# Kernel optimization log

Hardware: AMD Instinct MI355X
Metric: run time of the kernel (lower is better)

## Reference

```python
import jax, jax.numpy as jnp
import numpy as np

N = 50000
E = 800000
EL = 100000
IN_CH = 33
HID = 64
OUT = 128
NTYPES = 311
EMB = 16
COMB = IN_CH - 1 + EMB  # 48


def setup_inputs() -> dict:
    key = jax.random.key(0)
    ks = jax.random.split(key, 24)
    # x: col 0 = node type (integer-valued float), rest = float features
    types = jax.random.randint(ks[0], (N, 1), 0, NTYPES).astype(jnp.float32)
    feats = jax.random.normal(ks[1], (N, IN_CH - 1), dtype=jnp.float32)
    x = jnp.concatenate([types, feats], axis=1)
    edge_index = jax.random.randint(ks[2], (2, E), 0, N, dtype=jnp.int32)
    edge_label_index = jax.random.randint(ks[3], (2, EL), 0, N, dtype=jnp.int32)
    s = 0.05
    inp = {
        'x': x, 'edge_index': edge_index, 'edge_label_index': edge_label_index,
        'emb': jax.random.normal(ks[4], (NTYPES, EMB)) * s,
        'W1': jax.random.normal(ks[5], (COMB, 4 * HID)) * s,
        'a_src1': jax.random.normal(ks[6], (4, HID)) * s,
        'a_dst1': jax.random.normal(ks[7], (4, HID)) * s,
        'b1': jnp.zeros((4 * HID,)),
        'W2': jax.random.normal(ks[8], (4 * HID, 2 * 2 * HID)) * s,
        'a_src2': jax.random.normal(ks[9], (2, 2 * HID)) * s,
        'a_dst2': jax.random.normal(ks[10], (2, 2 * HID)) * s,
        'b2': jnp.zeros((2 * 2 * HID,)),
        'W3': jax.random.normal(ks[11], (4 * HID, OUT)) * s,
        'a_src3': jax.random.normal(ks[12], (1, OUT)) * s,
        'a_dst3': jax.random.normal(ks[13], (1, OUT)) * s,
        'b3': jnp.zeros((OUT,)),
        'Wl1': jax.random.normal(ks[14], (2 * OUT, HID)) * s,
        'bl1': jnp.zeros((HID,)),
        'Wl2': jax.random.normal(ks[15], (HID, 1)) * s,
        'bl2': jnp.zeros((1,)),
        'trans_bias': jax.random.normal(ks[16], (NTYPES, NTYPES)) * s,
    }
    return inp


def _gat(h_in, src, dst, W, a_src, a_dst, b, heads, d_out):
    # linear transform, per-head split
    h = (h_in @ W).reshape(N, heads, d_out)                      # [N,H,D]
    al_s = jnp.einsum('nhd,hd->nh', h, a_src)                    # [N,H]
    al_d = jnp.einsum('nhd,hd->nh', h, a_dst)
    logits = jax.nn.leaky_relu(al_s[src] + al_d[dst], 0.2)       # [E,H]
    m = jax.ops.segment_max(logits, dst, num_segments=N)
    m = jnp.where(jnp.isfinite(m), m, 0.0)
    e = jnp.exp(logits - m[dst])
    denom = jax.ops.segment_sum(e, dst, num_segments=N)
    alpha = e / (denom[dst] + 1e-16)                             # [E,H]
    msg = h[src] * alpha[:, :, None]                             # [E,H,D]
    out = jax.ops.segment_sum(msg, dst, num_segments=N)          # [N,H,D]
    return out.reshape(N, heads * d_out) + b


def reference(x, edge_index, edge_label_index, emb, W1, a_src1, a_dst1, b1,
              W2, a_src2, a_dst2, b2, W3, a_src3, a_dst3, b3,
              Wl1, bl1, Wl2, bl2, trans_bias):
    node_types = x[:, 0].astype(jnp.int32)
    x_comb = jnp.concatenate([emb[node_types], x[:, 1:]], axis=1)  # [N,48]
    # add self loops (PyG GATConv default)
    loops = jnp.arange(N, dtype=edge_index.dtype)
    ei = jnp.concatenate([edge_index, jnp.stack([loops, loops])], axis=1)
    src, dst = ei[0], ei[1]
    z = jax.nn.elu(_gat(x_comb, src, dst, W1, a_src1, a_dst1, b1, 4, HID))
    z = jax.nn.elu(_gat(z, src, dst, W2, a_src2, a_dst2, b2, 2, 2 * HID))
    z = _gat(z, src, dst, W3, a_src3, a_dst3, b3, 1, OUT)
    # decode
    ls, ld = edge_label_index[0], edge_label_index[1]
    ef = jnp.concatenate([z[ls], z[ld]], axis=1)                  # [EL,2*OUT]
    h = jax.nn.relu(ef @ Wl1 + bl1)
    base = h @ Wl2 + bl2                                          # [EL,1]
    bias = trans_bias[node_types[ls], node_types[ld]][:, None]
    return base + bias
```

## Files before the change

kernel.cpp:

```cpp
#include <hip/hip_runtime.h>
#include <hip/hip_bf16.h>

#define NN 50000
#define EE 800000
#define ELN 100000
#define ETOT (EE + NN)
#define NT 311

#define NBUCK ((NN + 127) >> 7)
#define BCAP 3072
#define CHUNK 8192

typedef _Float16 f16;
typedef f16 f16x8 __attribute__((ext_vector_type(8)));
typedef f16 f16x4 __attribute__((ext_vector_type(4)));
typedef f16 f16x2 __attribute__((ext_vector_type(2)));
typedef float f32x4 __attribute__((ext_vector_type(4)));

__global__ __launch_bounds__(256) void k_prepatt(const float* __restrict__ x,
                                                 const float* __restrict__ emb,
                                                 const float* __restrict__ a1ps,
                                                 const float* __restrict__ a1pd,
                                                 f16* __restrict__ xc,
                                                 int* __restrict__ ntypes,
                                                 float* __restrict__ als,
                                                 float* __restrict__ ald)
{
    int gid = blockIdx.x * 256 + threadIdx.x;
    int n = gid >> 6, lane = gid & 63;
    if (n >= NN) return;
    int tpe = (int)x[(size_t)n * 33];
    tpe = tpe < 0 ? 0 : (tpe > NT - 1 ? NT - 1 : tpe);
    if (lane == 0) ntypes[n] = tpe;
    float v;
    if (lane < 16)      v = emb[tpe * 16 + lane];
    else if (lane < 48) v = x[(size_t)n * 33 + 1 + (lane - 16)];
    else                v = 0.f;
    f16 hv = (f16)v;
    xc[(size_t)n * 64 + lane] = hv;
    float xv = (float)hv;
    float ps[4], pd[4];
    #pragma unroll
    for (int h = 0; h < 4; ++h) {
        ps[h] = xv * a1ps[h * 64 + lane];
        pd[h] = xv * a1pd[h * 64 + lane];
    }
    #pragma unroll
    for (int off = 32; off > 0; off >>= 1) {
        #pragma unroll
        for (int h = 0; h < 4; ++h) {
            ps[h] += __shfl_xor(ps[h], off, 64);
            pd[h] += __shfl_xor(pd[h], off, 64);
        }
    }
    if (lane == 0) {
        #pragma unroll
        for (int h = 0; h < 4; ++h) {
            als[n * 4 + h] = ps[h];
            ald[n * 4 + h] = pd[h];
        }
    }
}

__global__ __launch_bounds__(256) void k_cvtall(const float* __restrict__ W1,
                                                const float* __restrict__ W2,
                                                const float* __restrict__ W3,
                                                const float* __restrict__ Wl1,
                                                f16* __restrict__ Wt1,
                                                f16* __restrict__ Wt2,
                                                f16* __restrict__ Wt3,
                                                f16* __restrict__ Wtl)
{
    int idx = blockIdx.x * 256 + threadIdx.x;
    if (idx < 16384) {
        int h = idx >> 12, c = (idx >> 6) & 63, k = idx & 63;
        Wt1[idx] = (k < 48) ? (f16)W1[(size_t)k * 256 + h * 64 + c] : (f16)0.f;
    } else if (idx < 81920) {
        int i = idx - 16384;
        int c = i >> 8, k = i & 255;
        Wt2[i] = (f16)W2[(size_t)k * 256 + c];
    } else if (idx < 114688) {
        int i = idx - 81920;
        int c = i >> 8, k = i & 255;
        Wt3[i] = (f16)W3[(size_t)k * 128 + c];
    } else if (idx < 131072) {
        int i = idx - 114688;
        int c = i >> 8, k = i & 255;
        Wtl[i] = (f16)Wl1[(size_t)k * 64 + c];
    }
}

__global__ __launch_bounds__(256) void k_pre1(const float* __restrict__ W1,
                                              const float* __restrict__ as1,
                                              const float* __restrict__ ad1,
                                              float* __restrict__ a1ps,
                                              float* __restrict__ a1pd)
{
    int t = threadIdx.x;
    int h = t >> 6, k = t & 63;
    float ss = 0.f, sd = 0.f;
    if (k < 48) {
        for (int d = 0; d < 64; ++d) {
            float w = W1[(size_t)k * 256 + h * 64 + d];
            ss += w * as1[h * 64 + d];
            sd += w * ad1[h * 64 + d];
        }
    }
    a1ps[t] = ss;
    a1pd[t] = sd;
}

__global__ __launch_bounds__(256) void k_bucket(const int* __restrict__ ei,
                                                int* __restrict__ bcur,
                                                int2* __restrict__ bbuf)
{
    __shared__ int hist[NBUCK];
    __shared__ int gbase[NBUCK];
    const int t = threadIdx.x;
    for (int i = t; i < NBUCK; i += 256) hist[i] = 0;
    __syncthreads();
    const int e0 = blockIdx.x * CHUNK;
    const int eend = min(e0 + CHUNK, ETOT);
    for (int e = e0 + t; e < eend; e += 256) {
        int dst = (e < EE) ? ei[EE + e] : (e - EE);
        atomicAdd(&hist[dst >> 7], 1);
    }
    __syncthreads();
    for (int i = t; i < NBUCK; i += 256) {
        int c = hist[i];
        gbase[i] = c ? atomicAdd(&bcur[i], c) : 0;
        hist[i] = 0;
    }
    __syncthreads();
    for (int e = e0 + t; e < eend; e += 256) {
        int src, dst;
        if (e < EE) { src = ei[e]; dst = ei[EE + e]; }
        else        { src = e - EE; dst = src; }
        int b = dst >> 7;
        int pos = gbase[b] + atomicAdd(&hist[b], 1);
        if (pos < BCAP)
            bbuf[(size_t)b * BCAP + pos] = make_int2(src, dst);
    }
}

__global__ __launch_bounds__(512) void k_bscan(const int* __restrict__ bcur,
                                               int* __restrict__ boff)
{
    __shared__ int s[512];
    int t = threadIdx.x;
    int v = (t < NBUCK) ? min(bcur[t], BCAP) : 0;
    s[t] = v;
    __syncthreads();
    #pragma unroll
    for (int off = 1; off < 512; off <<= 1) {
        int u = (t >= off) ? s[t - off] : 0;
        __syncthreads();
        s[t] += u;
        __syncthreads();
    }
    if (t < NBUCK) boff[t] = s[t] - v;
    if (t == NBUCK - 1) boff[NBUCK] = s[t];
}

__global__ __launch_bounds__(256) void k_csrb(const int* __restrict__ bcur,
                                              const int* __restrict__ boff,
                                              const int2* __restrict__ bbuf,
                                              int* __restrict__ rowptr,
                                              int* __restrict__ csr,
                                              int* __restrict__ dstarr)
{
    __shared__ int nh[128];
    __shared__ int loff[128];
    __shared__ int ncur[128];
    __shared__ int ssrc[BCAP];
    __shared__ int sdst[BCAP];
    const int b = blockIdx.x;
    const int t = threadIdx.x;
    const int n0 = b << 7;
    const int cnt = min(bcur[b], BCAP);
    const int base = boff[b];
    const size_t bb = (size_t)b * BCAP;
    if (t < 128) { nh[t] = 0; ncur[t] = 0; }
    __syncthreads();
    for (int i = t; i < cnt; i += 256)
        atomicAdd(&nh[bbuf[bb + i].y - n0], 1);
    __syncthreads();
    int myc = (t < 128) ? nh[t] : 0;
    #pragma unroll
    for (int off = 1; off < 128; off <<= 1) {
        int u = (t >= off && t < 128) ? nh[t - off] : 0;
        __syncthreads();
        if (t < 128) nh[t] += u;
        __syncthreads();
    }
    if (t < 128) {
        int ex = nh[t] - myc;
        loff[t] = ex;
        int n = n0 + t;
        if (n < NN) rowptr[n] = base + ex;
    }
    __syncthreads();
    for (int i = t; i < cnt; i += 256) {
        int2 p = bbuf[bb + i];
        int ln = p.y - n0;
        int pos = loff[ln] + atomicAdd(&ncur[ln], 1);
        ssrc[pos] = p.x;
        sdst[pos] = p.y;
    }
    __syncthreads();
    for (int i = t; i < cnt; i += 256) {
        csr[base + i]    = ssrc[i];
        dstarr[base + i] = sdst[i];
    }
    if (b == 0 && t == 0) rowptr[NN] = boff[NBUCK];
}

template<int K, int CN, int H>
__global__ __launch_bounds__(256) void k_gemmh(const f16* __restrict__ A,
                                               const f16* __restrict__ Wt,
                                               f16* __restrict__ O,
                                               int nrows,
                                               const float* __restrict__ asrc,
                                               const float* __restrict__ adst,
                                               float* __restrict__ als,
                                               float* __restrict__ ald)
{
    constexpr int LDA = 40;
    __shared__ f16 As[64 * LDA];
    __shared__ f16 Bs[64 * LDA];
    const int t = threadIdx.x;
    const int w = t >> 6;
    const int lane = t & 63;
    const int m = lane & 15;
    const int quad = lane >> 4;
    const int row0 = blockIdx.x * 64;
    const int col0 = blockIdx.y * 64;
    const int r_st = t >> 2;
    const int seg  = (t & 3) * 8;
    f32x4 acc[4] = {{0.f,0.f,0.f,0.f},{0.f,0.f,0.f,0.f},{0.f,0.f,0.f,0.f},{0.f,0.f,0.f,0.f}};
    for (int k0 = 0; k0 < K; k0 += 32) {
        int gr = row0 + r_st;
        f16x8 av = {0,0,0,0,0,0,0,0};
        if (gr < nrows) av = *(const f16x8*)&A[(size_t)gr * K + k0 + seg];
        *(f16x8*)&As[r_st * LDA + seg] = av;
        f16x8 bv = *(const f16x8*)&Wt[(size_t)(col0 + r_st) * K + k0 + seg];
        *(f16x8*)&Bs[r_st * LDA + seg] = bv;
        __syncthreads();
        f16x8 af = *(const f16x8*)&As[(w * 16 + m) * LDA + quad * 8];
        #pragma unroll
        for (int g = 0; g < 4; ++g) {
            f16x8 bf = *(const f16x8*)&Bs[(g * 16 + m) * LDA + quad * 8];
            acc[g] = __builtin_amdgcn_mfma_f32_16x16x32_f16(af, bf, acc[g], 0, 0, 0);
        }
        __syncthreads();
    }
    #pragma unroll
    for (int g = 0; g < 4; ++g) {
        #pragma unroll
        for (int reg = 0; reg < 4; ++reg) {
            int gr = row0 + w * 16 + quad * 4 + reg;
            int gc = col0 + g * 16 + m;
            if (gr < nrows) O[(size_t)gr * CN + gc] = (f16)acc[g][reg];
        }
    }
    if constexpr (H > 0) {
        constexpr int D = CN / H;
        const int head = col0 / D;
        float ps[4] = {}, pd[4] = {};
        #pragma unroll
        for (int g = 0; g < 4; ++g) {
            int col = col0 + g * 16 + m;
            float a_s = asrc[col], a_d = adst[col];
            #pragma unroll
            for (int reg = 0; reg < 4; ++reg) {
                ps[reg] += acc[g][reg] * a_s;
                pd[reg] += acc[g][reg] * a_d;
            }
        }
        #pragma unroll
        for (int off = 1; off < 16; off <<= 1) {
            #pragma unroll
            for (int reg = 0; reg < 4; ++reg) {
                ps[reg] += __shfl_xor(ps[reg], off, 64);
                pd[reg] += __shfl_xor(pd[reg], off, 64);
            }
        }
        if (m == 0) {
            #pragma unroll
            for (int reg = 0; reg < 4; ++reg) {
                int gr = row0 + w * 16 + quad * 4 + reg;
                if (gr < nrows) {
                    atomicAdd(&als[gr * H + head], ps[reg]);
                    atomicAdd(&ald[gr * H + head], pd[reg]);
                }
            }
        }
    }
}

__global__ __launch_bounds__(256) void k_gemm1h(const f16* __restrict__ A,
                                                const f16* __restrict__ Wt1,
                                                const float* __restrict__ bias,
                                                f16* __restrict__ O,
                                                int nrows)
{
    constexpr int LDA = 40;
    __shared__ f16 As[64 * LDA];
    __shared__ f16 Bs[64 * LDA];
    const int t = threadIdx.x;
    const int w = t >> 6;
    const int lane = t & 63;
    const int m = lane & 15;
    const int quad = lane >> 4;
    const int row0 = blockIdx.x * 64;
    const int head = blockIdx.y;
    const int r_st = t >> 2;
    const int seg  = (t & 3) * 8;
    f32x4 acc[4] = {{0.f,0.f,0.f,0.f},{0.f,0.f,0.f,0.f},{0.f,0.f,0.f,0.f},{0.f,0.f,0.f,0.f}};
    for (int k0 = 0; k0 < 64; k0 += 32) {
        int gr = row0 + r_st;
        f16x8 av = {0,0,0,0,0,0,0,0};
        if (gr < nrows) av = *(const f16x8*)&A[(size_t)gr * 256 + head * 64 + k0 + seg];
        *(f16x8*)&As[r_st * LDA + seg] = av;
        f16x8 bv = *(const f16x8*)&Wt1[(size_t)head * 4096 + (size_t)r_st * 64 + k0 + seg];
        *(f16x8*)&Bs[r_st * LDA + seg] = bv;
        __syncthreads();
        f16x8 af = *(const f16x8*)&As[(w * 16 + m) * LDA + quad * 8];
        #pragma unroll
        for (int g = 0; g < 4; ++g) {
            f16x8 bf = *(const f16x8*)&Bs[(g * 16 + m) * LDA + quad * 8];
            acc[g] = __builtin_amdgcn_mfma_f32_16x16x32_f16(af, bf, acc[g], 0, 0, 0);
        }
        __syncthreads();
    }
    #pragma unroll
    for (int g = 0; g < 4; ++g) {
        #pragma unroll
        for (int reg = 0; reg < 4; ++reg) {
            int gr = row0 + w * 16 + quad * 4 + reg;
            int col = head * 64 + g * 16 + m;
            if (gr < nrows) {
                float v = acc[g][reg] + bias[col];
                v = v > 0.f ? v : (__expf(v) - 1.f);
                O[(size_t)gr * 256 + col] = (f16)v;
            }
        }
    }
}

template<int H>
__global__ __launch_bounds__(256) void k_ew(const int* __restrict__ csr,
                                            const int* __restrict__ dstarr,
                                            const float* __restrict__ als,
                                            const float* __restrict__ ald,
                                            float* __restrict__ earr)
{
    int i = blockIdx.x * 256 + threadIdx.x;
    if (i >= ETOT) return;
    int s = csr[i], d = dstarr[i];
    #pragma unroll
    for (int hh = 0; hh < H; ++hh) {
        float l = als[s * H + hh] + ald[d * H + hh];
        l = l > 0.f ? l : 0.2f * l;
        earr[(size_t)i * H + hh] = __expf(fminf(l, 80.f));
    }
}

__global__ __launch_bounds__(256) void k_aggx(const int* __restrict__ rowptr,
                                              const int* __restrict__ csr,
                                              const float* __restrict__ earr,
                                              const f16* __restrict__ xc,
                                              f16* __restrict__ xagg)
{
    int gid = blockIdx.x * 256 + threadIdx.x;
    int n = gid >> 6, lane = gid & 63;
    if (n >= NN) return;
    int p  = lane >> 5;
    int cb = (lane & 31) * 2;
    int r0 = rowptr[n], r1 = rowptr[n + 1];
    float a0[2] = {}, a1[2] = {}, a2[2] = {}, a3[2] = {};
    float d0 = 0.f, d1 = 0.f, d2 = 0.f, d3 = 0.f;
    int i = r0;
    for (; i + 4 <= r1; i += 4) {
        int i0 = i + p, i1 = i + 2 + p;
        int s0 = csr[i0], s1 = csr[i1];
        float4 e0 = *(const float4*)&earr[(size_t)i0 * 4];
        float4 e1 = *(const float4*)&earr[(size_t)i1 * 4];
        f16x2 x0 = *(const f16x2*)&xc[(size_t)s0 * 64 + cb];
        f16x2 x1 = *(const f16x2*)&xc[(size_t)s1 * 64 + cb];
        #pragma unroll
        for (int j = 0; j < 2; ++j) {
            float v0 = (float)x0[j], v1 = (float)x1[j];
            a0[j] += e0.x * v0 + e1.x * v1;
            a1[j] += e0.y * v0 + e1.y * v1;
            a2[j] += e0.z * v0 + e1.z * v1;
            a3[j] += e0.w * v0 + e1.w * v1;
        }
        d0 += e0.x + e1.x; d1 += e0.y + e1.y;
        d2 += e0.z + e1.z; d3 += e0.w + e1.w;
    }
    for (; i < r1; i += 2) {
        int ii = i + p;
        bool v = ii < r1;
        int s0 = csr[v ? ii : r0];
        float4 e0 = *(const float4*)&earr[(size_t)(v ? ii : r0) * 4];
        if (!v) { e0.x = 0.f; e0.y = 0.f; e0.z = 0.f; e0.w = 0.f; }
        f16x2 x0 = *(const f16x2*)&xc[(size_t)s0 * 64 + cb];
        #pragma unroll
        for (int j = 0; j < 2; ++j) {
            float v0 = (float)x0[j];
            a0[j] += e0.x * v0; a1[j] += e0.y * v0;
            a2[j] += e0.z * v0; a3[j] += e0.w * v0;
        }
        d0 += e0.x; d1 += e0.y; d2 += e0.z; d3 += e0.w;
    }
    #pragma unroll
    for (int j = 0; j < 2; ++j) {
        a0[j] += __shfl_xor(a0[j], 32, 64);
        a1[j] += __shfl_xor(a1[j], 32, 64);
        a2[j] += __shfl_xor(a2[j], 32, 64);
        a3[j] += __shfl_xor(a3[j], 32, 64);
    }
    d0 += __shfl_xor(d0, 32, 64);
    d1 += __shfl_xor(d1, 32, 64);
    d2 += __shfl_xor(d2, 32, 64);
    d3 += __shfl_xor(d3, 32, 64);
    if (p == 0) {
        float i0 = 1.f / d0, i1 = 1.f / d1, i2 = 1.f / d2, i3 = 1.f / d3;
        size_t base = (size_t)n * 256 + cb;
        f16x2 o0 = {(f16)(a0[0] * i0), (f16)(a0[1] * i0)};
        f16x2 o1 = {(f16)(a1[0] * i1), (f16)(a1[1] * i1)};
        f16x2 o2 = {(f16)(a2[0] * i2), (f16)(a2[1] * i2)};
        f16x2 o3 = {(f16)(a3[0] * i3), (f16)(a3[1] * i3)};
        *(f16x2*)&xagg[base]       = o0;
        *(f16x2*)&xagg[base + 64]  = o1;
        *(f16x2*)&xagg[base + 128] = o2;
        *(f16x2*)&xagg[base + 192] = o3;
    }
}

__global__ __launch_bounds__(256) void k_agg2f(const int* __restrict__ rowptr,
                                               const int* __restrict__ csr,
                                               const float* __restrict__ earr,
                                               const f16* __restrict__ h,
                                               const float* __restrict__ bias,
                                               f16* __restrict__ z)
{
    int gid = blockIdx.x * 256 + threadIdx.x;
    int n = gid >> 6, lane = gid & 63;
    if (n >= NN) return;
    int p  = lane >> 5;
    int cb = (lane & 31) * 8;
    int head = cb >> 7;
    int r0 = rowptr[n], r1 = rowptr[n + 1];
    float a[8] = {};
    float den = 0.f;
    int i = r0;
    for (; i + 8 <= r1; i += 8) {
        int i0 = i + p, i1 = i + 2 + p, i2 = i + 4 + p, i3 = i + 6 + p;
        int s0 = csr[i0], s1 = csr[i1], s2 = csr[i2], s3 = csr[i3];
        float e0 = earr[(size_t)i0 * 2 + head];
        float e1 = earr[(size_t)i1 * 2 + head];
        float e2 = earr[(size_t)i2 * 2 + head];
        float e3 = earr[(size_t)i3 * 2 + head];
        f16x8 h0 = *(const f16x8*)&h[(size_t)s0 * 256 + cb];
        f16x8 h1 = *(const f16x8*)&h[(size_t)s1 * 256 + cb];
        f16x8 h2 = *(const f16x8*)&h[(size_t)s2 * 256 + cb];
        f16x8 h3 = *(const f16x8*)&h[(size_t)s3 * 256 + cb];
        #pragma unroll
        for (int j = 0; j < 8; ++j)
            a[j] += e0 * (float)h0[j] + e1 * (float)h1[j]
                  + e2 * (float)h2[j] + e3 * (float)h3[j];
        den += e0 + e1 + e2 + e3;
    }
    for (; i < r1; i += 2) {
        int ii = i + p;
        bool v = ii < r1;
        int s0 = csr[v ? ii : r0];
        float e0 = v ? earr[(size_t)ii * 2 + head] : 0.f;
        f16x8 h0 = *(const f16x8*)&h[(size_t)s0 * 256 + cb];
        #pragma unroll
        for (int j = 0; j < 8; ++j) a[j] += e0 * (float)h0[j];
        den += e0;
    }
    #pragma unroll
    for (int j = 0; j < 8; ++j) a[j] += __shfl_xor(a[j], 32, 64);
    den += __shfl_xor(den, 32, 64);
    if (p == 0) {
        float inv = 1.f / den;
        f16x8 o;
        #pragma unroll
        for (int j = 0; j < 8; ++j) {
            float v = a[j] * inv + bias[cb + j];
            v = v > 0.f ? v : (__expf(v) - 1.f);
            o[j] = (f16)v;
        }
        *(f16x8*)&z[(size_t)n * 256 + cb] = o;
    }
}

__global__ __launch_bounds__(256) void k_agg3(const int* __restrict__ rowptr,
                                              const int* __restrict__ csr,
                                              const float* __restrict__ earr,
                                              const f16* __restrict__ h,
                                              const float* __restrict__ bias,
                                              f16* __restrict__ z)
{
    int gid = blockIdx.x * 256 + threadIdx.x;
    int n = gid >> 6, lane = gid & 63;
    if (n >= NN) return;
    int p  = lane >> 4;
    int cb = (lane & 15) * 8;
    int r0 = rowptr[n], r1 = rowptr[n + 1];
    float a[8] = {};
    float den = 0.f;
    int i = r0;
    for (; i + 8 <= r1; i += 8) {
        int i0 = i + p, i1 = i + 4 + p;
        int s0 = csr[i0], s1 = csr[i1];
        float e0 = earr[i0], e1 = earr[i1];
        f16x8 h0 = *(const f16x8*)&h[(size_t)s0 * 128 + cb];
        f16x8 h1 = *(const f16x8*)&h[(size_t)s1 * 128 + cb];
        #pragma unroll
        for (int j = 0; j < 8; ++j)
            a[j] += e0 * (float)h0[j] + e1 * (float)h1[j];
        den += e0 + e1;
    }
    for (; i < r1; i += 4) {
        int ii = i + p;
        bool v = ii < r1;
        int s0 = csr[v ? ii : r0];
        float e0 = v ? earr[ii] : 0.f;
        f16x8 h0 = *(const f16x8*)&h[(size_t)s0 * 128 + cb];
        #pragma unroll
        for (int j = 0; j < 8; ++j) a[j] += e0 * (float)h0[j];
        den += e0;
    }
    #pragma unroll
    for (int j = 0; j < 8; ++j) {
        a[j] += __shfl_xor(a[j], 16, 64);
        a[j] += __shfl_xor(a[j], 32, 64);
    }
    den += __shfl_xor(den, 16, 64);
    den += __shfl_xor(den, 32, 64);
    if (lane < 16) {
        float inv = 1.f / den;
        f16x8 o;
        #pragma unroll
        for (int j = 0; j < 8; ++j)
            o[j] = (f16)(a[j] * inv + bias[cb + j]);
        *(f16x8*)&z[(size_t)n * 128 + cb] = o;
    }
}

#define DLDA 264
__global__ __launch_bounds__(256) void k_decm(const f16* __restrict__ z3,
                                              const int* __restrict__ eli,
                                              const int* __restrict__ ntypes,
                                              const f16* __restrict__ Wtl,
                                              const float* __restrict__ bl1,
                                              const float* __restrict__ Wl2,
                                              const float* __restrict__ bl2,
                                              const float* __restrict__ tb,
                                              float* __restrict__ out)
{
    __shared__ f16 As[64 * DLDA];
    __shared__ int sls[64], sld[64];
    const int t = threadIdx.x;
    const int e0 = blockIdx.x * 64;
    if (t < 64) {
        int e = e0 + t;
        sls[t] = (e < ELN) ? eli[e] : 0;
        sld[t] = (e < ELN) ? eli[ELN + e] : 0;
    }
    __syncthreads();
    {
        int r = t & 63;
        int seg = t >> 6;
        int base = seg * 64;
        int node = (base < 128) ? sls[r] : sld[r];
        int zoff = base & 127;
        #pragma unroll
        for (int j = 0; j < 8; ++j) {
            f16x8 v = *(const f16x8*)&z3[(size_t)node * 128 + zoff + j * 8];
            *(f16x8*)&As[r * DLDA + base + j * 8] = v;
        }
    }
    __syncthreads();
    const int w = t >> 6;
    const int lane = t & 63;
    const int m = lane & 15;
    const int quad = lane >> 4;
    f32x4 acc[4] = {{0.f,0.f,0.f,0.f},{0.f,0.f,0.f,0.f},{0.f,0.f,0.f,0.f},{0.f,0.f,0.f,0.f}};
    for (int k0 = 0; k0 < 256; k0 += 32) {
        f16x8 af = *(const f16x8*)&As[(w * 16 + m) * DLDA + k0 + quad * 8];
        #pragma unroll
        for (int g = 0; g < 4; ++g) {
            f16x8 bf = *(const f16x8*)&Wtl[(size_t)(g * 16 + m) * 256 + k0 + quad * 8];
            acc[g] = __builtin_amdgcn_mfma_f32_16x16x32_f16(af, bf, acc[g], 0, 0, 0);
        }
    }
    float s[4] = {0.f, 0.f, 0.f, 0.f};
    #pragma unroll
    for (int g = 0; g < 4; ++g) {
        int col = g * 16 + m;
        float b = bl1[col], wv = Wl2[col];
        #pragma unroll
        for (int reg = 0; reg < 4; ++reg) {
            float hv = fmaxf(acc[g][reg] + b, 0.f);
            s[reg] += hv * wv;
        }
    }
    #pragma unroll
    for (int off = 1; off < 16; off <<= 1) {
        #pragma unroll
        for (int reg = 0; reg < 4; ++reg) s[reg] += __shfl_xor(s[reg], off, 64);
    }
    if (m == 0) {
        float b2v = bl2[0];
        #pragma unroll
        for (int reg = 0; reg < 4; ++reg) {
            int r = w * 16 + quad * 4 + reg;
            int e = e0 + r;
            if (e < ELN) {
                out[e] = s[reg] + b2v +
                         tb[(size_t)ntypes[sls[r]] * NT + ntypes[sld[r]]];
            }
        }
    }
}

extern "C" void kernel_launch(void* const* d_in, const int* in_sizes, int n_in,
                              void* d_out, int out_size, void* d_ws, size_t ws_size,
                              hipStream_t stream)
{
    const float* x   = (const float*)d_in[0];
    const int*   ei  = (const int*)d_in[1];
    const int*   eli = (const int*)d_in[2];
    const float* emb = (const float*)d_in[3];
    const float* W1  = (const float*)d_in[4];
    const float* as1 = (const float*)d_in[5];
    const float* ad1 = (const float*)d_in[6];
    const float* b1  = (const float*)d_in[7];
    const float* W2  = (const float*)d_in[8];
    const float* as2 = (const float*)d_in[9];
    const float* ad2 = (const float*)d_in[10];
    const float* b2  = (const float*)d_in[11];
    const float* W3  = (const float*)d_in[12];
    const float* as3 = (const float*)d_in[13];
    const float* ad3 = (const float*)d_in[14];
    const float* b3  = (const float*)d_in[15];
    const float* Wl1 = (const float*)d_in[16];
    const float* bl1 = (const float*)d_in[17];
    const float* Wl2 = (const float*)d_in[18];
    const float* bl2 = (const float*)d_in[19];
    const float* tb  = (const float*)d_in[20];
    float* out = (float*)d_out;

    char* ws = (char*)d_ws;
    size_t off = 0;
    auto alloc = [&](size_t bytes) { size_t o = off; off = (off + bytes + 255) & ~(size_t)255; return o; };
    int*   ntypes = (int*)  (ws + alloc((size_t)NN * 4));
    f16*   xc16   = (f16*)  (ws + alloc((size_t)NN * 64 * 2));
    int*   rowptr = (int*)  (ws + alloc((size_t)(NN + 1) * 4));
    int*   csr    = (int*)  (ws + alloc((size_t)ETOT * 4));
    int*   dstarr = (int*)  (ws + alloc((size_t)ETOT * 4));
    int*   bcur   = (int*)  (ws + alloc((size_t)(NBUCK + 1) * 4));
    int*   boff   = (int*)  (ws + alloc((size_t)(NBUCK + 1) * 4));
    float* scores = (float*)(ws + alloc((size_t)NN * 14 * 4));
    float* als1 = scores;
    float* ald1 = scores + (size_t)NN * 4;
    float* als2 = scores + (size_t)NN * 8;
    float* ald2 = scores + (size_t)NN * 10;
    float* als3 = scores + (size_t)NN * 12;
    float* ald3 = scores + (size_t)NN * 13;
    float* earr   = (float*)(ws + alloc((size_t)ETOT * 4 * 4));
    f16*   h16    = (f16*)  (ws + alloc((size_t)NN * 256 * 2));
    f16*   z16    = (f16*)  (ws + alloc((size_t)NN * 256 * 2));
    f16*   Wt1    = (f16*)  (ws + alloc((size_t)4 * 64 * 64 * 2));
    f16*   Wt2    = (f16*)  (ws + alloc((size_t)256 * 256 * 2));
    f16*   Wt3    = (f16*)  (ws + alloc((size_t)128 * 256 * 2));
    f16*   Wtl    = (f16*)  (ws + alloc((size_t)64 * 256 * 2));
    float* a1ps   = (float*)(ws + alloc(256 * 4));
    float* a1pd   = (float*)(ws + alloc(256 * 4));

    int2* bbuf = (int2*)earr;

    hipMemsetAsync(bcur, 0, (size_t)(NBUCK + 1) * 4, stream);
    hipMemsetAsync(als2, 0, (size_t)NN * 6 * 4, stream);

    const int gE   = (ETOT + 255) / 256;
    const int RB   = (NN + 63) / 64;
    const int gW1  = (NN + 3) / 4;

    k_pre1<<<1, 256, 0, stream>>>(W1, as1, ad1, a1ps, a1pd);
    k_prepatt<<<gW1, 256, 0, stream>>>(x, emb, a1ps, a1pd, xc16, ntypes, als1, ald1);
    k_cvtall<<<(131072 + 255) / 256, 256, 0, stream>>>(W1, W2, W3, Wl1, Wt1, Wt2, Wt3, Wtl);

    k_bucket<<<(ETOT + CHUNK - 1) / CHUNK, 256, 0, stream>>>(ei, bcur, bbuf);
    k_bscan <<<1, 512, 0, stream>>>(bcur, boff);
    k_csrb  <<<NBUCK, 256, 0, stream>>>(bcur, boff, bbuf, rowptr, csr, dstarr);

    k_ew<4><<<gE, 256, 0, stream>>>(csr, dstarr, als1, ald1, earr);
    k_aggx<<<gW1, 256, 0, stream>>>(rowptr, csr, earr, xc16, h16 );
    k_gemm1h<<<dim3(RB, 4), 256, 0, stream>>>(h16 , Wt1, b1, z16, NN);

    k_gemmh<256, 256, 2><<<dim3(RB, 4), 256, 0, stream>>>(z16, Wt2, h16, NN, as2, ad2, als2, ald2);
    k_ew<2><<<gE, 256, 0, stream>>>(csr, dstarr, als2, ald2, earr);
    k_agg2f<<<gW1, 256, 0, stream>>>(rowptr, csr, earr, h16, b2, z16);

    k_gemmh<256, 128, 1><<<dim3(RB, 2), 256, 0, stream>>>(z16, Wt3, h16, NN, as3, ad3, als3, ald3);
    k_ew<1><<<gE, 256, 0, stream>>>(csr, dstarr, als3, ald3, earr);
    k_agg3<<<gW1, 256, 0, stream>>>(rowptr, csr, earr, h16, b3, z16);

    k_decm<<<(ELN + 63) / 64, 256, 0, stream>>>(z16, eli, ntypes, Wtl, bl1, Wl2, bl2, tb, out);
}
```

Before: 417.0 us.

## Fuse edge-weight computation into aggregation kernels and drop dst array

Removes the three separate per-edge exp kernels and the materialized edge-weight array. Each aggregation kernel now computes leaky-relu/exp attention weights on the fly from the per-node source and destination scores. The CSR build no longer writes a destination array, and the edge bucket buffer gets its own allocation. The aggregation loops are also unrolled deeper to keep more gathers in flight. In exchange, the exp is recomputed redundantly across lanes and the gather loops use more registers.

```diff
diff --git a/kernel.cpp b/kernel.cpp
--- a/kernel.cpp
+++ b/kernel.cpp
@@ -16,6 +16,12 @@
 typedef f16 f16x4 __attribute__((ext_vector_type(4)));
 typedef f16 f16x2 __attribute__((ext_vector_type(2)));
 typedef float f32x4 __attribute__((ext_vector_type(4)));
+
+__device__ __forceinline__ float edge_alpha(float l)
+{
+    l = l > 0.f ? l : 0.2f * l;
+    return __expf(fminf(l, 80.f));
+}
 
 __global__ __launch_bounds__(256) void k_prepatt(const float* __restrict__ x,
                                                  const float* __restrict__ emb,
@@ -166,14 +172,12 @@
                                               const int* __restrict__ boff,
                                               const int2* __restrict__ bbuf,
                                               int* __restrict__ rowptr,
-                                              int* __restrict__ csr,
-                                              int* __restrict__ dstarr)
+                                              int* __restrict__ csr)
 {
     __shared__ int nh[128];
     __shared__ int loff[128];
     __shared__ int ncur[128];
     __shared__ int ssrc[BCAP];
-    __shared__ int sdst[BCAP];
     const int b = blockIdx.x;
     const int t = threadIdx.x;
     const int n0 = b << 7;
@@ -205,13 +209,10 @@
         int ln = p.y - n0;
         int pos = loff[ln] + atomicAdd(&ncur[ln], 1);
         ssrc[pos] = p.x;
-        sdst[pos] = p.y;
-    }
-    __syncthreads();
-    for (int i = t; i < cnt; i += 256) {
-        csr[base + i]    = ssrc[i];
-        dstarr[base + i] = sdst[i];
-    }
+    }
+    __syncthreads();
+    for (int i = t; i < cnt; i += 256)
+        csr[base + i] = ssrc[i];
     if (b == 0 && t == 0) rowptr[NN] = boff[NBUCK];
 }
 
@@ -348,27 +349,10 @@
     }
 }
 
-template<int H>
-__global__ __launch_bounds__(256) void k_ew(const int* __restrict__ csr,
-                                            const int* __restrict__ dstarr,
-                                            const float* __restrict__ als,
-                                            const float* __restrict__ ald,
-                                            float* __restrict__ earr)
-{
-    int i = blockIdx.x * 256 + threadIdx.x;
-    if (i >= ETOT) return;
-    int s = csr[i], d = dstarr[i];
-    #pragma unroll
-    for (int hh = 0; hh < H; ++hh) {
-        float l = als[s * H + hh] + ald[d * H + hh];
-        l = l > 0.f ? l : 0.2f * l;
-        earr[(size_t)i * H + hh] = __expf(fminf(l, 80.f));
-    }
-}
-
 __global__ __launch_bounds__(256) void k_aggx(const int* __restrict__ rowptr,
                                               const int* __restrict__ csr,
-                                              const float* __restrict__ earr,
+                                              const float* __restrict__ als,
+                                              const float* __restrict__ ald,
                                               const f16* __restrict__ xc,
                                               f16* __restrict__ xagg)
 {
@@ -378,33 +362,48 @@
     int p  = lane >> 5;
     int cb = (lane & 31) * 2;
     int r0 = rowptr[n], r1 = rowptr[n + 1];
+    float4 dl = *(const float4*)&ald[(size_t)n * 4];
     float a0[2] = {}, a1[2] = {}, a2[2] = {}, a3[2] = {};
     float d0 = 0.f, d1 = 0.f, d2 = 0.f, d3 = 0.f;
     int i = r0;
-    for (; i + 4 <= r1; i += 4) {
-        int i0 = i + p, i1 = i + 2 + p;
-        int s0 = csr[i0], s1 = csr[i1];
-        float4 e0 = *(const float4*)&earr[(size_t)i0 * 4];
-        float4 e1 = *(const float4*)&earr[(size_t)i1 * 4];
-        f16x2 x0 = *(const f16x2*)&xc[(size_t)s0 * 64 + cb];
-        f16x2 x1 = *(const f16x2*)&xc[(size_t)s1 * 64 + cb];
-        #pragma unroll
-        for (int j = 0; j < 2; ++j) {
-            float v0 = (float)x0[j], v1 = (float)x1[j];
-            a0[j] += e0.x * v0 + e1.x * v1;
-            a1[j] += e0.y * v0 + e1.y * v1;
-            a2[j] += e0.z * v0 + e1.z * v1;
-            a3[j] += e0.w * v0 + e1.w * v1;
-        }
-        d0 += e0.x + e1.x; d1 += e0.y + e1.y;
-        d2 += e0.z + e1.z; d3 += e0.w + e1.w;
+    for (; i + 8 <= r1; i += 8) {
+        int s[4]; float4 A[4]; f16x2 xv[4]; float4 e[4];
+        #pragma unroll
+        for (int k = 0; k < 4; ++k) s[k] = csr[i + 2 * k + p];
+        #pragma unroll
+        for (int k = 0; k < 4; ++k) xv[k] = *(const f16x2*)&xc[(size_t)s[k] * 64 + cb];
+        #pragma unroll
+        for (int k = 0; k < 4; ++k) A[k] = *(const float4*)&als[(size_t)s[k] * 4];
+        #pragma unroll
+        for (int k = 0; k < 4; ++k) {
+            e[k].x = edge_alpha(A[k].x + dl.x);
+            e[k].y = edge_alpha(A[k].y + dl.y);
+            e[k].z = edge_alpha(A[k].z + dl.z);
+            e[k].w = edge_alpha(A[k].w + dl.w);
+        }
+        #pragma unroll
+        for (int k = 0; k < 4; ++k) {
+            #pragma unroll
+            for (int j = 0; j < 2; ++j) {
+                float v0 = (float)xv[k][j];
+                a0[j] += e[k].x * v0;
+                a1[j] += e[k].y * v0;
+                a2[j] += e[k].z * v0;
+                a3[j] += e[k].w * v0;
+            }
+            d0 += e[k].x; d1 += e[k].y; d2 += e[k].z; d3 += e[k].w;
+        }
     }
     for (; i < r1; i += 2) {
         int ii = i + p;
         bool v = ii < r1;
         int s0 = csr[v ? ii : r0];
-        float4 e0 = *(const float4*)&earr[(size_t)(v ? ii : r0) * 4];
-        if (!v) { e0.x = 0.f; e0.y = 0.f; e0.z = 0.f; e0.w = 0.f; }
+        float4 A0 = *(const float4*)&als[(size_t)s0 * 4];
+        float4 e0;
+        e0.x = v ? edge_alpha(A0.x + dl.x) : 0.f;
+        e0.y = v ? edge_alpha(A0.y + dl.y) : 0.f;
+        e0.z = v ? edge_alpha(A0.z + dl.z) : 0.f;
+        e0.w = v ? edge_alpha(A0.w + dl.w) : 0.f;
         f16x2 x0 = *(const f16x2*)&xc[(size_t)s0 * 64 + cb];
         #pragma unroll
         for (int j = 0; j < 2; ++j) {
@@ -441,7 +440,8 @@
 
 __global__ __launch_bounds__(256) void k_agg2f(const int* __restrict__ rowptr,
                                                const int* __restrict__ csr,
-                                               const float* __restrict__ earr,
+                                               const float* __restrict__ als,
+                                               const float* __restrict__ ald,
                                                const f16* __restrict__ h,
                                                const float* __restrict__ bias,
                                                f16* __restrict__ z)
@@ -451,33 +451,47 @@
     if (n >= NN) return;
     int p  = lane >> 5;
     int cb = (lane & 31) * 8;
-    int head = cb >> 7;
+    int head = (lane & 31) >> 4;
     int r0 = rowptr[n], r1 = rowptr[n + 1];
+    float dd = ald[(size_t)n * 2 + head];
     float a[8] = {};
     float den = 0.f;
     int i = r0;
+    for (; i + 16 <= r1; i += 16) {
+        int s[8]; f16x8 hv[8]; float e[8];
+        #pragma unroll
+        for (int k = 0; k < 8; ++k) s[k] = csr[i + 2 * k + p];
+        #pragma unroll
+        for (int k = 0; k < 8; ++k) hv[k] = *(const f16x8*)&h[(size_t)s[k] * 256 + cb];
+        #pragma unroll
+        for (int k = 0; k < 8; ++k) e[k] = edge_alpha(als[(size_t)s[k] * 2 + head] + dd);
+        #pragma unroll
+        for (int k = 0; k < 8; ++k) {
+            den += e[k];
+            #pragma unroll
+            for (int j = 0; j < 8; ++j) a[j] += e[k] * (float)hv[k][j];
+        }
+    }
     for (; i + 8 <= r1; i += 8) {
-        int i0 = i + p, i1 = i + 2 + p, i2 = i + 4 + p, i3 = i + 6 + p;
-        int s0 = csr[i0], s1 = csr[i1], s2 = csr[i2], s3 = csr[i3];
-        float e0 = earr[(size_t)i0 * 2 + head];
-        float e1 = earr[(size_t)i1 * 2 + head];
-        float e2 = earr[(size_t)i2 * 2 + head];
-        float e3 = earr[(size_t)i3 * 2 + head];
-        f16x8 h0 = *(const f16x8*)&h[(size_t)s0 * 256 + cb];
-        f16x8 h1 = *(const f16x8*)&h[(size_t)s1 * 256 + cb];
-        f16x8 h2 = *(const f16x8*)&h[(size_t)s2 * 256 + cb];
-        f16x8 h3 = *(const f16x8*)&h[(size_t)s3 * 256 + cb];
-        #pragma unroll
-        for (int j = 0; j < 8; ++j)
-            a[j] += e0 * (float)h0[j] + e1 * (float)h1[j]
-                  + e2 * (float)h2[j] + e3 * (float)h3[j];
-        den += e0 + e1 + e2 + e3;
+        int s[4]; f16x8 hv[4]; float e[4];
+        #pragma unroll
+        for (int k = 0; k < 4; ++k) s[k] = csr[i + 2 * k + p];
+        #pragma unroll
+        for (int k = 0; k < 4; ++k) hv[k] = *(const f16x8*)&h[(size_t)s[k] * 256 + cb];
+        #pragma unroll
+        for (int k = 0; k < 4; ++k) e[k] = edge_alpha(als[(size_t)s[k] * 2 + head] + dd);
+        #pragma unroll
+        for (int k = 0; k < 4; ++k) {
+            den += e[k];
+            #pragma unroll
+            for (int j = 0; j < 8; ++j) a[j] += e[k] * (float)hv[k][j];
+        }
     }
     for (; i < r1; i += 2) {
         int ii = i + p;
         bool v = ii < r1;
         int s0 = csr[v ? ii : r0];
-        float e0 = v ? earr[(size_t)ii * 2 + head] : 0.f;
+        float e0 = v ? edge_alpha(als[(size_t)s0 * 2 + head] + dd) : 0.f;
         f16x8 h0 = *(const f16x8*)&h[(size_t)s0 * 256 + cb];
         #pragma unroll
         for (int j = 0; j < 8; ++j) a[j] += e0 * (float)h0[j];
@@ -501,7 +515,8 @@
 
 __global__ __launch_bounds__(256) void k_agg3(const int* __restrict__ rowptr,
                                               const int* __restrict__ csr,
-                                              const float* __restrict__ earr,
+                                              const float* __restrict__ als,
+                                              const float* __restrict__ ald,
                                               const f16* __restrict__ h,
                                               const float* __restrict__ bias,
                                               f16* __restrict__ z)
@@ -512,25 +527,45 @@
     int p  = lane >> 4;
     int cb = (lane & 15) * 8;
     int r0 = rowptr[n], r1 = rowptr[n + 1];
+    float dd = ald[n];
     float a[8] = {};
     float den = 0.f;
     int i = r0;
+    for (; i + 16 <= r1; i += 16) {
+        int s[4]; f16x8 hv[4]; float e[4];
+        #pragma unroll
+        for (int k = 0; k < 4; ++k) s[k] = csr[i + 4 * k + p];
+        #pragma unroll
+        for (int k = 0; k < 4; ++k) hv[k] = *(const f16x8*)&h[(size_t)s[k] * 128 + cb];
+        #pragma unroll
+        for (int k = 0; k < 4; ++k) e[k] = edge_alpha(als[s[k]] + dd);
+        #pragma unroll
+        for (int k = 0; k < 4; ++k) {
+            den += e[k];
+            #pragma unroll
+            for (int j = 0; j < 8; ++j) a[j] += e[k] * (float)hv[k][j];
+        }
+    }
     for (; i + 8 <= r1; i += 8) {
-        int i0 = i + p, i1 = i + 4 + p;
-        int s0 = csr[i0], s1 = csr[i1];
-        float e0 = earr[i0], e1 = earr[i1];
-        f16x8 h0 = *(const f16x8*)&h[(size_t)s0 * 128 + cb];
-        f16x8 h1 = *(const f16x8*)&h[(size_t)s1 * 128 + cb];
-        #pragma unroll
-        for (int j = 0; j < 8; ++j)
-            a[j] += e0 * (float)h0[j] + e1 * (float)h1[j];
-        den += e0 + e1;
+        int s[2]; f16x8 hv[2]; float e[2];
+        #pragma unroll
+        for (int k = 0; k < 2; ++k) s[k] = csr[i + 4 * k + p];
+        #pragma unroll
+        for (int k = 0; k < 2; ++k) hv[k] = *(const f16x8*)&h[(size_t)s[k] * 128 + cb];
+        #pragma unroll
+        for (int k = 0; k < 2; ++k) e[k] = edge_alpha(als[s[k]] + dd);
+        #pragma unroll
+        for (int k = 0; k < 2; ++k) {
+            den += e[k];
+            #pragma unroll
+            for (int j = 0; j < 8; ++j) a[j] += e[k] * (float)hv[k][j];
+        }
     }
     for (; i < r1; i += 4) {
         int ii = i + p;
         bool v = ii < r1;
         int s0 = csr[v ? ii : r0];
-        float e0 = v ? earr[ii] : 0.f;
+        float e0 = v ? edge_alpha(als[s0] + dd) : 0.f;
         f16x8 h0 = *(const f16x8*)&h[(size_t)s0 * 128 + cb];
         #pragma unroll
         for (int j = 0; j < 8; ++j) a[j] += e0 * (float)h0[j];
@@ -664,7 +699,6 @@
     f16*   xc16   = (f16*)  (ws + alloc((size_t)NN * 64 * 2));
     int*   rowptr = (int*)  (ws + alloc((size_t)(NN + 1) * 4));
     int*   csr    = (int*)  (ws + alloc((size_t)ETOT * 4));
-    int*   dstarr = (int*)  (ws + alloc((size_t)ETOT * 4));
     int*   bcur   = (int*)  (ws + alloc((size_t)(NBUCK + 1) * 4));
     int*   boff   = (int*)  (ws + alloc((size_t)(NBUCK + 1) * 4));
     float* scores = (float*)(ws + alloc((size_t)NN * 14 * 4));
@@ -674,7 +708,7 @@
     float* ald2 = scores + (size_t)NN * 10;
     float* als3 = scores + (size_t)NN * 12;
     float* ald3 = scores + (size_t)NN * 13;
-    float* earr   = (float*)(ws + alloc((size_t)ETOT * 4 * 4));
+    int2*  bbuf   = (int2*) (ws + alloc((size_t)NBUCK * BCAP * 8));
     f16*   h16    = (f16*)  (ws + alloc((size_t)NN * 256 * 2));
     f16*   z16    = (f16*)  (ws + alloc((size_t)NN * 256 * 2));
     f16*   Wt1    = (f16*)  (ws + alloc((size_t)4 * 64 * 64 * 2));
@@ -684,12 +718,9 @@
     float* a1ps   = (float*)(ws + alloc(256 * 4));
     float* a1pd   = (float*)(ws + alloc(256 * 4));
 
-    int2* bbuf = (int2*)earr;
-
     hipMemsetAsync(bcur, 0, (size_t)(NBUCK + 1) * 4, stream);
     hipMemsetAsync(als2, 0, (size_t)NN * 6 * 4, stream);
 
-    const int gE   = (ETOT + 255) / 256;
     const int RB   = (NN + 63) / 64;
     const int gW1  = (NN + 3) / 4;
 
@@ -699,19 +730,16 @@
 
     k_bucket<<<(ETOT + CHUNK - 1) / CHUNK, 256, 0, stream>>>(ei, bcur, bbuf);
     k_bscan <<<1, 512, 0, stream>>>(bcur, boff);
-    k_csrb  <<<NBUCK, 256, 0, stream>>>(bcur, boff, bbuf, rowptr, csr, dstarr);
-
-    k_ew<4><<<gE, 256, 0, stream>>>(csr, dstarr, als1, ald1, earr);
-    k_aggx<<<gW1, 256, 0, stream>>>(rowptr, csr, earr, xc16, h16 );
+    k_csrb  <<<NBUCK, 256, 0, stream>>>(bcur, boff, bbuf, rowptr, csr);
+
+    k_aggx<<<gW1, 256, 0, stream>>>(rowptr, csr, als1, ald1, xc16, h16 );
     k_gemm1h<<<dim3(RB, 4), 256, 0, stream>>>(h16 , Wt1, b1, z16, NN);
 
     k_gemmh<256, 256, 2><<<dim3(RB, 4), 256, 0, stream>>>(z16, Wt2, h16, NN, as2, ad2, als2, ald2);
-    k_ew<2><<<gE, 256, 0, stream>>>(csr, dstarr, als2, ald2, earr);
-    k_agg2f<<<gW1, 256, 0, stream>>>(rowptr, csr, earr, h16, b2, z16);
+    k_agg2f<<<gW1, 256, 0, stream>>>(rowptr, csr, als2, ald2, h16, b2, z16);
 
     k_gemmh<256, 128, 1><<<dim3(RB, 2), 256, 0, stream>>>(z16, Wt3, h16, NN, as3, ad3, als3, ald3);
-    k_ew<1><<<gE, 256, 0, stream>>>(csr, dstarr, als3, ald3, earr);
-    k_agg3<<<gW1, 256, 0, stream>>>(rowptr, csr, earr, h16, b3, z16);
+    k_agg3<<<gW1, 256, 0, stream>>>(rowptr, csr, als3, ald3, h16, b3, z16);
 
     k_decm<<<(ELN + 63) / 64, 256, 0, stream>>>(z16, eli, ntypes, Wtl, bl1, Wl2, bl2, tb, out);
 }
```

After: 422.4 us. No clear change (+1.3%).
